# Optimization experiments

Hardware: AMD Instinct MI355X
Metric: run time of the kernel (lower is better)

Reference implementation:

```python
import jax, jax.numpy as jnp
import numpy as np
import math

D_MODEL = 1024
NUM_HEADS = 16
D_K = D_MODEL // NUM_HEADS
MAX_SEQ_LEN = 2048
THETA = 10000.0
BATCH = 2
SEQ = 2048


def setup_inputs() -> dict:
    key = jax.random.key(0)
    ks = jax.random.split(key, 5)
    std = math.sqrt(2.0 / (D_MODEL + D_MODEL))
    def w(k):
        return jnp.clip(std * jax.random.normal(k, (D_MODEL, D_MODEL), dtype=jnp.float32), -3 * std, 3 * std)
    return {
        "x": jax.random.normal(ks[0], (BATCH, SEQ, D_MODEL), dtype=jnp.float32),
        "token_positions": jnp.arange(SEQ, dtype=jnp.int32),
        "Wq": w(ks[1]),
        "Wk": w(ks[2]),
        "Wv": w(ks[3]),
        "Wo": w(ks[4]),
    }


def _rope_tables():
    inv_freq = 1.0 / THETA ** (jnp.arange(0, D_K, 2, dtype=jnp.float32) / D_K)  # [d_k/2]
    positions = jnp.arange(MAX_SEQ_LEN, dtype=jnp.float32)[:, None]             # [max_seq, 1]
    angles = positions * inv_freq                                               # [max_seq, d_k/2]
    return jnp.cos(angles), jnp.sin(angles)


def _apply_rope(x, cos, sin):
    # x: [..., seq, d_k]; cos/sin: [seq, d_k/2] (broadcast over leading dims)
    x1, x2 = x[..., ::2], x[..., 1::2]
    r1 = x1 * cos - x2 * sin
    r2 = x1 * sin + x2 * cos
    return jnp.stack((r1, r2), axis=-1).reshape(x.shape)


def reference(x, token_positions, Wq, Wk, Wv, Wo):
    B, S, D = x.shape
    def proj(W):
        y = jnp.einsum('bsd,od->bso', x, W)
        return y.reshape(B, S, NUM_HEADS, D_K).transpose(0, 2, 1, 3)  # [B,H,S,dk]
    q, k, v = proj(Wq), proj(Wk), proj(Wv)

    cos_t, sin_t = _rope_tables()
    cos, sin = cos_t[token_positions], sin_t[token_positions]  # [S, d_k/2]
    q = _apply_rope(q, cos, sin)
    k = _apply_rope(k, cos, sin)

    scores = jnp.einsum('bhqd,bhkd->bhqk', q, k) / math.sqrt(D_K)
    causal = jnp.tril(jnp.ones((S, S), dtype=bool))
    scores = jnp.where(causal, scores, -jnp.inf)
    attn = jax.nn.softmax(scores, axis=-1)
    out = jnp.einsum('bhqk,bhkd->bhqd', attn, v)
    out = out.transpose(0, 2, 1, 3).reshape(B, S, D)
    return jnp.einsum('bsd,od->bso', out, Wo)
```

## Files before the change

### kernel.cpp

```cpp
#include <hip/hip_runtime.h>
#include <hip/hip_bf16.h>


typedef __attribute__((ext_vector_type(8))) short short8;
typedef __attribute__((ext_vector_type(4))) float floatx4;

static __device__ __forceinline__ unsigned short f2bf(float f) {
  __hip_bfloat16 h = __float2bfloat16(f);
  return *(unsigned short*)&h;
}

static __device__ __forceinline__ unsigned int pk2bf(float a, float b) {
  unsigned int ua = __float_as_uint(a) + 0x8000u;
  unsigned int ub = __float_as_uint(b) + 0x8000u;
  return __builtin_amdgcn_perm(ub, ua, 0x07060302u);
}

static __device__ __forceinline__ float fexp2(float x) {
  float r;
  asm("v_exp_f32 %0, %1\n\ts_nop 0" : "=v"(r) : "v"(x));
  return r;
}

static __device__ __forceinline__ void gl2lds16(const unsigned short* g,
                                                unsigned short* l) {
  __builtin_amdgcn_global_load_lds(
      (const __attribute__((address_space(1))) void*)g,
      (__attribute__((address_space(3))) void*)l, 16, 0, 0);
}

__global__ __launch_bounds__(256) void cvt_all(
    const float4* __restrict__ x,  const float4* __restrict__ wq,
    const float4* __restrict__ wk, const float4* __restrict__ wv,
    const float4* __restrict__ wo,
    ushort4* __restrict__ xb,  ushort4* __restrict__ wqb,
    ushort4* __restrict__ wkb, ushort4* __restrict__ wvb,
    ushort4* __restrict__ wob,
    const int* __restrict__ tokpos,
    float* __restrict__ ctab, float* __restrict__ stab) {
  int t = blockIdx.y;
  int i = blockIdx.x * 256 + threadIdx.x;
  if (t == 5) {
    if (i < 65536) {
      int s = i >> 5, f = i & 31;
      float inv = expf(-9.210340371976184f * (float)(2 * f) / 64.0f);
      float ang = (float)tokpos[s] * inv;
      ctab[i] = cosf(ang);
      stab[i] = sinf(ang);
    }
    return;
  }
  const float4* s = (t == 0) ? x : (t == 1) ? wq : (t == 2) ? wk : (t == 3) ? wv : wo;
  ushort4* d = (t == 0) ? xb : (t == 1) ? wqb : (t == 2) ? wkb : (t == 3) ? wvb : wob;
  int n4 = (t == 0) ? 1048576 : 262144;
  if (i < n4) {
    float4 v = s[i];
    ushort4 o;
    o.x = f2bf(v.x); o.y = f2bf(v.y); o.z = f2bf(v.z); o.w = f2bf(v.w);
    d[i] = o;
  }
}

#define GEMM128_BODY(Aptr, Wptr, m0, n0)                                        \
  __shared__ __align__(16) unsigned short lA[2][128 * 64];                      \
  __shared__ __align__(16) unsigned short lB[2][128 * 64];                      \
  int tid = threadIdx.x;                                                        \
  int wave = tid >> 6, lane = tid & 63;                                         \
  int wm = wave >> 1, wn = wave & 1;                                            \
  int l15 = lane & 15, quad = lane >> 4;                                        \
  int srow = wave * 32 + (lane >> 3);                   \
  int sch = lane & 7;                                   \
  int fsw = l15 & 7;                                 \
  floatx4 acc[4][4];                                                            \
  _Pragma("unroll") for (int m = 0; m < 4; ++m)                                 \
      _Pragma("unroll") for (int n = 0; n < 4; ++n)                             \
          acc[m][n] = (floatx4){0.f, 0.f, 0.f, 0.f};                            \
                    \
  _Pragma("unroll") for (int p = 0; p < 4; ++p) {                               \
    int r = srow + p * 8;                                                       \
    int g = sch ^ (r & 7);                                                      \
    gl2lds16(Aptr + (size_t)(m0 + r) * 1024 + g * 8,                            \
             lA[0] + (wave * 32 + p * 8) * 64);                                 \
    gl2lds16(Wptr + (size_t)(n0 + r) * 1024 + g * 8,                            \
             lB[0] + (wave * 32 + p * 8) * 64);                                 \
  }                                                                             \
  _Pragma("unroll") for (int p = 0; p < 4; ++p) {                               \
    int r = srow + p * 8;                                                       \
    int g = sch ^ (r & 7);                                                      \
    gl2lds16(Aptr + (size_t)(m0 + r) * 1024 + 64 + g * 8,                       \
             lA[1] + (wave * 32 + p * 8) * 64);                                 \
    gl2lds16(Wptr + (size_t)(n0 + r) * 1024 + 64 + g * 8,                       \
             lB[1] + (wave * 32 + p * 8) * 64);                                 \
  }                                                                             \
  asm volatile("s_waitcnt vmcnt(8)" ::: "memory");               \
  __builtin_amdgcn_s_barrier();                                                 \
  for (int kt = 0; kt < 16; ++kt) {                                             \
    int cur = kt & 1;                                                           \
    _Pragma("unroll") for (int ks = 0; ks < 2; ++ks) {                          \
      short8 af[4], bf[4];                                                      \
      _Pragma("unroll") for (int m = 0; m < 4; ++m)                             \
          af[m] = *(const short8*)(lA[cur] + (wm * 64 + m * 16 + l15) * 64 +    \
                                   (((ks * 4 + quad) ^ fsw) * 8));              \
      _Pragma("unroll") for (int n = 0; n < 4; ++n)                             \
          bf[n] = *(const short8*)(lB[cur] + (wn * 64 + n * 16 + l15) * 64 +    \
                                   (((ks * 4 + quad) ^ fsw) * 8));              \
      _Pragma("unroll") for (int m = 0; m < 4; ++m)                             \
          _Pragma("unroll") for (int n = 0; n < 4; ++n)                         \
              acc[m][n] = __builtin_amdgcn_mfma_f32_16x16x32_bf16(              \
                  af[m], bf[n], acc[m][n], 0, 0, 0);                            \
    }                                                                           \
    if (kt == 15) break;                                                        \
    __builtin_amdgcn_s_barrier();                                      \
    if (kt < 14) {                                                              \
      _Pragma("unroll") for (int p = 0; p < 4; ++p) {                           \
        int r = srow + p * 8;                                                   \
        int g = sch ^ (r & 7);                                                  \
        gl2lds16(Aptr + (size_t)(m0 + r) * 1024 + (kt + 2) * 64 + g * 8,        \
                 lA[cur] + (wave * 32 + p * 8) * 64);                           \
        gl2lds16(Wptr + (size_t)(n0 + r) * 1024 + (kt + 2) * 64 + g * 8,        \
                 lB[cur] + (wave * 32 + p * 8) * 64);                           \
      }                                                                         \
      asm volatile("s_waitcnt vmcnt(8)" ::: "memory");        \
    } else {                                                                    \
      asm volatile("s_waitcnt vmcnt(0)" ::: "memory");         \
    }                                                                           \
    __builtin_amdgcn_s_barrier();                                      \
  }

__global__ __launch_bounds__(256) void qkv_mfma(
    const unsigned short* __restrict__ X,
    const unsigned short* __restrict__ Wq,
    const unsigned short* __restrict__ Wk,
    const unsigned short* __restrict__ Wv,
    const float* __restrict__ ctab, const float* __restrict__ stab,
    unsigned short* __restrict__ Qo, unsigned short* __restrict__ Ko,
    unsigned short* __restrict__ Vo) {
  int mat = blockIdx.z;
  const unsigned short* W = (mat == 0) ? Wq : ((mat == 1) ? Wk : Wv);
  unsigned short* Out = (mat == 0) ? Qo : ((mat == 1) ? Ko : Vo);
  int m0 = blockIdx.x * 128, n0 = blockIdx.y * 128;

  GEMM128_BODY(X, W, m0, n0)

#pragma unroll
  for (int n = 0; n < 4; ++n) {
    int col = n0 + wn * 64 + n * 16 + l15;
    int h = col >> 6;
    int d = col & 63;
    int pi = d >> 1;
    bool odd = (d & 1) != 0;
    size_t hb = (size_t)h * 2048 * 64;
#pragma unroll
    for (int m = 0; m < 4; ++m) {
      int row0 = m0 + wm * 64 + m * 16 + quad * 4;
      int b = row0 >> 11;
      int s0 = row0 & 2047;
      size_t base = (size_t)b * 16 * 2048 * 64 + hb;
      if (mat == 2) {
        ushort4 pv;
        pv.x = f2bf(acc[m][n][0]);
        pv.y = f2bf(acc[m][n][1]);
        pv.z = f2bf(acc[m][n][2]);
        pv.w = f2bf(acc[m][n][3]);
        *(ushort4*)(Out + base + (size_t)d * 2048 + s0) = pv;
      } else {
#pragma unroll
        for (int i = 0; i < 4; ++i) {
          int s = s0 + i;
          float v = acc[m][n][i];
          float p = __shfl_xor(v, 1);
          float c = ctab[s * 32 + pi];
          float sn = stab[s * 32 + pi];
          float res = odd ? fmaf(p, sn, v * c) : fmaf(v, c, -p * sn);
          if (mat == 0) res *= 0.1803368801111204f;
          Out[base + (size_t)s * 64 + d] = f2bf(res);
        }
      }
    }
  }
}

__global__ __launch_bounds__(256) void oproj_mfma(
    const unsigned short* __restrict__ A, const unsigned short* __restrict__ Wo,
    float* __restrict__ Out) {
  __shared__ __align__(16) unsigned short lA[2][64 * 64];
  __shared__ __align__(16) unsigned short lB[2][128 * 64];
  int tid = threadIdx.x;
  int wave = tid >> 6, lane = tid & 63;
  int l15 = lane & 15, quad = lane >> 4;
  int rsub = lane >> 3, sch = lane & 7;
  int fsw = l15 & 7;
  int m0 = blockIdx.x * 64, n0 = blockIdx.y * 128;

  floatx4 acc[4][2];
#pragma unroll
  for (int m = 0; m < 4; ++m)
#pragma unroll
    for (int n = 0; n < 2; ++n) acc[m][n] = (floatx4){0.f, 0.f, 0.f, 0.f};

#pragma unroll
  for (int kp = 0; kp < 2; ++kp) {
#pragma unroll
    for (int p = 0; p < 2; ++p) {
      int r = wave * 16 + p * 8 + rsub;
      int g = sch ^ (r & 7);
      gl2lds16(A + (size_t)(m0 + r) * 1024 + kp * 64 + g * 8,
               lA[kp] + (wave * 16 + p * 8) * 64);
    }
#pragma unroll
    for (int p = 0; p < 4; ++p) {
      int r = wave * 32 + p * 8 + rsub;
      int g = sch ^ (r & 7);
      gl2lds16(Wo + (size_t)(n0 + r) * 1024 + kp * 64 + g * 8,
               lB[kp] + (wave * 32 + p * 8) * 64);
    }
  }
  asm volatile("s_waitcnt vmcnt(6)" ::: "memory");
  __builtin_amdgcn_s_barrier();

  for (int kt = 0; kt < 16; ++kt) {
    int cur = kt & 1;
#pragma unroll
    for (int ks = 0; ks < 2; ++ks) {
      int slot = ((ks * 4 + quad) ^ fsw) * 8;
      short8 af[4], bf[2];
#pragma unroll
      for (int m = 0; m < 4; ++m)
        af[m] = *(const short8*)(lA[cur] + (m * 16 + l15) * 64 + slot);
#pragma unroll
      for (int n = 0; n < 2; ++n)
        bf[n] = *(const short8*)(lB[cur] + (wave * 32 + n * 16 + l15) * 64 + slot);
#pragma unroll
      for (int m = 0; m < 4; ++m)
#pragma unroll
        for (int n = 0; n < 2; ++n)
          acc[m][n] = __builtin_amdgcn_mfma_f32_16x16x32_bf16(
              af[m], bf[n], acc[m][n], 0, 0, 0);
    }
    if (kt == 15) break;
    __builtin_amdgcn_s_barrier();
    if (kt < 14) {
#pragma unroll
      for (int p = 0; p < 2; ++p) {
        int r = wave * 16 + p * 8 + rsub;
        int g = sch ^ (r & 7);
        gl2lds16(A + (size_t)(m0 + r) * 1024 + (kt + 2) * 64 + g * 8,
                 lA[cur] + (wave * 16 + p * 8) * 64);
      }
#pragma unroll
      for (int p = 0; p < 4; ++p) {
        int r = wave * 32 + p * 8 + rsub;
        int g = sch ^ (r & 7);
        gl2lds16(Wo + (size_t)(n0 + r) * 1024 + (kt + 2) * 64 + g * 8,
                 lB[cur] + (wave * 32 + p * 8) * 64);
      }
      asm volatile("s_waitcnt vmcnt(6)" ::: "memory");
    } else {
      asm volatile("s_waitcnt vmcnt(0)" ::: "memory");
    }
    __builtin_amdgcn_s_barrier();
  }

#pragma unroll
  for (int m = 0; m < 4; ++m) {
#pragma unroll
    for (int n = 0; n < 2; ++n) {
      int col = n0 + wave * 32 + n * 16 + l15;
#pragma unroll
      for (int i = 0; i < 4; ++i) {
        int row = m0 + m * 16 + quad * 4 + i;
        Out[(size_t)row * 1024 + col] = acc[m][n][i];
      }
    }
  }
}

#define LPS 72

__global__ __launch_bounds__(256) void attn_flash(
    const unsigned short* __restrict__ Q, const unsigned short* __restrict__ K,
    const unsigned short* __restrict__ Vt, unsigned short* __restrict__ Oc) {
  __shared__ __align__(16) unsigned short lK[64 * 64];
  __shared__ __align__(16) unsigned short lV[64 * 64];
  __shared__ unsigned short lP[4][16 * LPS];

  int tid = threadIdx.x;
  int wave = tid >> 6, lane = tid & 63;
  int l15 = lane & 15, quad = lane >> 4;

  int xb_ = blockIdx.x;
  int yb_ = blockIdx.y;
  int jb = yb_ >> 3, ib = yb_ & 7;
  int qtile;
  if (jb == 0)      qtile = xb_;
  else if (jb == 1) qtile = 31 - xb_;
  else if (jb == 2) qtile = (15 - xb_) & 31;
  else              qtile = (16 + xb_) & 31;
  int bh = ib * 4 + jb;

  size_t base = (size_t)bh * 2048 * 64;
  int qbase = qtile * 64;

  const unsigned short* qrow = Q + base + (size_t)(qbase + wave * 16 + l15) * 64;
  short8 qb0 = *(const short8*)(qrow + quad * 8);
  short8 qb1 = *(const short8*)(qrow + 32 + quad * 8);

  floatx4 o[4];
  float m_i = -1e30f, l_i = 0.f;
#pragma unroll
  for (int n = 0; n < 4; ++n) o[n] = (floatx4){0.f, 0.f, 0.f, 0.f};

  int r0 = tid >> 3, g = tid & 7;
  int r1 = r0 + 32;
  int e0 = g * 8;
  int sl = (g ^ (r0 & 7)) * 8;
  int fsw = l15 & 7;
  int c0 = (quad ^ fsw) * 8;
  int c1 = ((quad + 4) ^ fsw) * 8;

  const unsigned short* kp = K + base;
  const unsigned short* vp = Vt + base;
  short8 pk0 = *(const short8*)(kp + r0 * 64 + e0);
  short8 pk1 = *(const short8*)(kp + r1 * 64 + e0);
  short8 pv0 = *(const short8*)(vp + (size_t)r0 * 2048 + e0);
  short8 pv1 = *(const short8*)(vp + (size_t)r1 * 2048 + e0);

  for (int kt = 0; kt <= qtile; ++kt) {
    __syncthreads();
    *(short8*)(lK + r0 * 64 + sl) = pk0;
    *(short8*)(lK + r1 * 64 + sl) = pk1;
    *(short8*)(lV + r0 * 64 + sl) = pv0;
    *(short8*)(lV + r1 * 64 + sl) = pv1;
    __syncthreads();

    if (kt < qtile) {
      const unsigned short* kn = K + base + (size_t)(kt + 1) * 4096;
      const unsigned short* vn = Vt + base + (kt + 1) * 64;
      pk0 = *(const short8*)(kn + r0 * 64 + e0);
      pk1 = *(const short8*)(kn + r1 * 64 + e0);
      pv0 = *(const short8*)(vn + (size_t)r0 * 2048 + e0);
      pv1 = *(const short8*)(vn + (size_t)r1 * 2048 + e0);
    }

    float sc[4][4];
#pragma unroll
    for (int sub = 0; sub < 4; ++sub) {
      const unsigned short* kr = lK + (sub * 16 + l15) * 64;
      short8 a0 = *(const short8*)(kr + c0);
      short8 a1 = *(const short8*)(kr + c1);
      floatx4 s = {0.f, 0.f, 0.f, 0.f};
      s = __builtin_amdgcn_mfma_f32_16x16x32_bf16(a0, qb0, s, 0, 0, 0);
      s = __builtin_amdgcn_mfma_f32_16x16x32_bf16(a1, qb1, s, 0, 0, 0);
#pragma unroll
      for (int i = 0; i < 4; ++i) sc[sub][i] = s[i];
    }

    if (kt == qtile) {
      int qin = wave * 16 + l15;
#pragma unroll
      for (int sub = 0; sub < 4; ++sub)
#pragma unroll
        for (int i = 0; i < 4; ++i)
          if (sub * 16 + quad * 4 + i > qin) sc[sub][i] = -1e30f;
    }

    float mb = sc[0][0];
#pragma unroll
    for (int sub = 0; sub < 4; ++sub)
#pragma unroll
      for (int i = 0; i < 4; ++i) mb = fmaxf(mb, sc[sub][i]);
    mb = fmaxf(mb, __shfl_xor(mb, 16));
    mb = fmaxf(mb, __shfl_xor(mb, 32));

    float mn = fmaxf(m_i, mb);
    float al = fexp2(m_i - mn);
    m_i = mn;
    float rs = 0.f;
#pragma unroll
    for (int sub = 0; sub < 4; ++sub)
#pragma unroll
      for (int i = 0; i < 4; ++i) {
        float p = fexp2(sc[sub][i] - mn);
        sc[sub][i] = p;
        rs += p;
      }
    rs += __shfl_xor(rs, 16);
    rs += __shfl_xor(rs, 32);
    l_i = l_i * al + rs;

#pragma unroll
    for (int n = 0; n < 4; ++n) {
      o[n][0] *= al; o[n][1] *= al; o[n][2] *= al; o[n][3] *= al;
    }

    unsigned short* pw = lP[wave] + l15 * LPS;
#pragma unroll
    for (int sub = 0; sub < 4; ++sub) {
      uint2 w;
      w.x = pk2bf(sc[sub][0], sc[sub][1]);
      w.y = pk2bf(sc[sub][2], sc[sub][3]);
      *(uint2*)(pw + sub * 16 + quad * 4) = w;
    }

    const unsigned short* pr = lP[wave] + l15 * LPS + quad * 8;
    short8 pa0 = *(const short8*)(pr);
    short8 pa1 = *(const short8*)(pr + 32);

#pragma unroll
    for (int n = 0; n < 4; ++n) {
      const unsigned short* vr = lV + (n * 16 + l15) * 64;
      short8 vb0 = *(const short8*)(vr + c0);
      short8 vb1 = *(const short8*)(vr + c1);
      o[n] = __builtin_amdgcn_mfma_f32_16x16x32_bf16(vb0, pa0, o[n], 0, 0, 0);
      o[n] = __builtin_amdgcn_mfma_f32_16x16x32_bf16(vb1, pa1, o[n], 0, 0, 0);
    }
  }

  int b = bh >> 4, h = bh & 15;
  float inv = 1.f / l_i;
  int s = qbase + wave * 16 + l15;
  size_t orow = (size_t)(b * 2048 + s) * 1024 + h * 64;
#pragma unroll
  for (int n = 0; n < 4; ++n) {
    uint2 ov;
    ov.x = pk2bf(o[n][0] * inv, o[n][1] * inv);
    ov.y = pk2bf(o[n][2] * inv, o[n][3] * inv);
    *(uint2*)(Oc + orow + n * 16 + quad * 4) = ov;
  }
}

extern "C" void kernel_launch(void* const* d_in, const int* in_sizes, int n_in,
                              void* d_out, int out_size, void* d_ws, size_t ws_size,
                              hipStream_t stream) {
  const float* x  = (const float*)d_in[0];
  const int* tokpos = (const int*)d_in[1];
  const float* Wq = (const float*)d_in[2];
  const float* Wk = (const float*)d_in[3];
  const float* Wv = (const float*)d_in[4];
  const float* Wo = (const float*)d_in[5];
  float* out = (float*)d_out;

  float* ws = (float*)d_ws;
  float* ctab = ws;
  float* stab = ctab + 65536;
  unsigned short* u = (unsigned short*)(stab + 65536);
  unsigned short* Qb  = u;
  unsigned short* Kb  = Qb + 4194304;
  unsigned short* Vb  = Kb + 4194304;
  unsigned short* Oc  = Vb + 4194304;
  unsigned short* xb  = Oc + 4194304;
  unsigned short* Wqb = xb + 4194304;
  unsigned short* Wkb = Wqb + 1048576;
  unsigned short* Wvb = Wkb + 1048576;
  unsigned short* Wob = Wvb + 1048576;

  cvt_all<<<dim3(4096, 6), 256, 0, stream>>>(
      (const float4*)x, (const float4*)Wq, (const float4*)Wk,
      (const float4*)Wv, (const float4*)Wo,
      (ushort4*)xb, (ushort4*)Wqb, (ushort4*)Wkb, (ushort4*)Wvb, (ushort4*)Wob,
      tokpos, ctab, stab);

  qkv_mfma<<<dim3(32, 8, 3), 256, 0, stream>>>(
      xb, Wqb, Wkb, Wvb, ctab, stab, Qb, Kb, Vb);
  attn_flash<<<dim3(32, 32), 256, 0, stream>>>(Qb, Kb, Vb, Oc);
  oproj_mfma<<<dim3(64, 8), 256, 0, stream>>>(Oc, Wob, out);
}
```

Measured before the change: 186.3 us.

## Pair complementary causal query tiles per attention block to share K/V loads

Each attention block now processes two query tiles, tA and 31-tA, that share the same (batch, head). The K/V tiles staged in LDS are reused by both, and every block does the same total amount of causal work. The grid shrinks from 1024 blocks to 512, and launch bounds now request 2 blocks per SM. In exchange, register pressure roughly doubles because two sets of accumulators and Q fragments are live, and parallelism drops to 512 blocks.

```diff
diff --git a/kernel.cpp b/kernel.cpp
--- a/kernel.cpp
+++ b/kernel.cpp
@@ -277,38 +277,119 @@
 
 #define LPS 72
 
-__global__ __launch_bounds__(256) void attn_flash(
+static __device__ __forceinline__ void qk_step(
+    const unsigned short* lK, int l15, int c0, int c1,
+    short8 q0, short8 q1, floatx4 (&sc)[4]) {
+#pragma unroll
+  for (int sub = 0; sub < 4; ++sub) {
+    const unsigned short* kr = lK + (sub * 16 + l15) * 64;
+    short8 a0 = *(const short8*)(kr + c0);
+    short8 a1 = *(const short8*)(kr + c1);
+    floatx4 s = {0.f, 0.f, 0.f, 0.f};
+    s = __builtin_amdgcn_mfma_f32_16x16x32_bf16(a0, q0, s, 0, 0, 0);
+    s = __builtin_amdgcn_mfma_f32_16x16x32_bf16(a1, q1, s, 0, 0, 0);
+    sc[sub] = s;
+  }
+}
+
+static __device__ __forceinline__ void sm_step(
+    floatx4 (&sc)[4], float& m_i, float& l_i, floatx4 (&o)[4],
+    bool diag, int qin, int quad) {
+  if (diag) {
+#pragma unroll
+    for (int sub = 0; sub < 4; ++sub)
+#pragma unroll
+      for (int i = 0; i < 4; ++i)
+        if (sub * 16 + quad * 4 + i > qin) sc[sub][i] = -1e30f;
+  }
+  float mb = sc[0][0];
+#pragma unroll
+  for (int sub = 0; sub < 4; ++sub)
+#pragma unroll
+    for (int i = 0; i < 4; ++i) mb = fmaxf(mb, sc[sub][i]);
+  mb = fmaxf(mb, __shfl_xor(mb, 16));
+  mb = fmaxf(mb, __shfl_xor(mb, 32));
+
+  float mn = fmaxf(m_i, mb);
+  float al = fexp2(m_i - mn);
+  m_i = mn;
+  float rs = 0.f;
+#pragma unroll
+  for (int sub = 0; sub < 4; ++sub)
+#pragma unroll
+    for (int i = 0; i < 4; ++i) {
+      float p = fexp2(sc[sub][i] - mn);
+      sc[sub][i] = p;
+      rs += p;
+    }
+  rs += __shfl_xor(rs, 16);
+  rs += __shfl_xor(rs, 32);
+  l_i = l_i * al + rs;
+#pragma unroll
+  for (int n = 0; n < 4; ++n) {
+    o[n][0] *= al; o[n][1] *= al; o[n][2] *= al; o[n][3] *= al;
+  }
+}
+
+static __device__ __forceinline__ void pv_step(
+    const floatx4 (&sc)[4], floatx4 (&o)[4], unsigned short* lPw,
+    const unsigned short* lV, int l15, int quad, int c0, int c1) {
+  unsigned short* pw = lPw + l15 * LPS;
+#pragma unroll
+  for (int sub = 0; sub < 4; ++sub) {
+    uint2 w;
+    w.x = pk2bf(sc[sub][0], sc[sub][1]);
+    w.y = pk2bf(sc[sub][2], sc[sub][3]);
+    *(uint2*)(pw + sub * 16 + quad * 4) = w;
+  }
+  const unsigned short* pr = lPw + l15 * LPS + quad * 8;
+  short8 pa0 = *(const short8*)(pr);
+  short8 pa1 = *(const short8*)(pr + 32);
+#pragma unroll
+  for (int n = 0; n < 4; ++n) {
+    const unsigned short* vr = lV + (n * 16 + l15) * 64;
+    short8 vb0 = *(const short8*)(vr + c0);
+    short8 vb1 = *(const short8*)(vr + c1);
+    o[n] = __builtin_amdgcn_mfma_f32_16x16x32_bf16(vb0, pa0, o[n], 0, 0, 0);
+    o[n] = __builtin_amdgcn_mfma_f32_16x16x32_bf16(vb1, pa1, o[n], 0, 0, 0);
+  }
+}
+
+__global__ __launch_bounds__(256, 2) void attn_flash(
     const unsigned short* __restrict__ Q, const unsigned short* __restrict__ K,
     const unsigned short* __restrict__ Vt, unsigned short* __restrict__ Oc) {
   __shared__ __align__(16) unsigned short lK[64 * 64];
   __shared__ __align__(16) unsigned short lV[64 * 64];
-  __shared__ unsigned short lP[4][16 * LPS];
+  __shared__ unsigned short lP[8][16 * LPS];
 
   int tid = threadIdx.x;
   int wave = tid >> 6, lane = tid & 63;
   int l15 = lane & 15, quad = lane >> 4;
 
-  int xb_ = blockIdx.x;
-  int yb_ = blockIdx.y;
-  int jb = yb_ >> 3, ib = yb_ & 7;
-  int qtile;
-  if (jb == 0)      qtile = xb_;
-  else if (jb == 1) qtile = 31 - xb_;
-  else if (jb == 2) qtile = (15 - xb_) & 31;
-  else              qtile = (16 + xb_) & 31;
-  int bh = ib * 4 + jb;
+  int id = blockIdx.x;
+  int rest = id >> 3;
+  int pair = rest >> 2;
+  int bh = (id & 7) * 4 + (rest & 3);
+  int tA = pair;
+  int tB = 31 - pair;
+  int NT = tB + 1;
 
   size_t base = (size_t)bh * 2048 * 64;
-  int qbase = qtile * 64;
-
-  const unsigned short* qrow = Q + base + (size_t)(qbase + wave * 16 + l15) * 64;
-  short8 qb0 = *(const short8*)(qrow + quad * 8);
-  short8 qb1 = *(const short8*)(qrow + 32 + quad * 8);
-
-  floatx4 o[4];
-  float m_i = -1e30f, l_i = 0.f;
-#pragma unroll
-  for (int n = 0; n < 4; ++n) o[n] = (floatx4){0.f, 0.f, 0.f, 0.f};
+
+  const unsigned short* qrowA = Q + base + (size_t)(tA * 64 + wave * 16 + l15) * 64;
+  const unsigned short* qrowB = Q + base + (size_t)(tB * 64 + wave * 16 + l15) * 64;
+  short8 qA0 = *(const short8*)(qrowA + quad * 8);
+  short8 qA1 = *(const short8*)(qrowA + 32 + quad * 8);
+  short8 qB0 = *(const short8*)(qrowB + quad * 8);
+  short8 qB1 = *(const short8*)(qrowB + 32 + quad * 8);
+
+  floatx4 oA[4], oB[4];
+  float mA_i = -1e30f, lA_i = 0.f, mB_i = -1e30f, lB_i = 0.f;
+#pragma unroll
+  for (int n = 0; n < 4; ++n) {
+    oA[n] = (floatx4){0.f, 0.f, 0.f, 0.f};
+    oB[n] = (floatx4){0.f, 0.f, 0.f, 0.f};
+  }
 
   int r0 = tid >> 3, g = tid & 7;
   int r1 = r0 + 32;
@@ -325,7 +406,11 @@
   short8 pv0 = *(const short8*)(vp + (size_t)r0 * 2048 + e0);
   short8 pv1 = *(const short8*)(vp + (size_t)r1 * 2048 + e0);
 
-  for (int kt = 0; kt <= qtile; ++kt) {
+  int qin = wave * 16 + l15;
+
+  for (int kt = 0; kt < NT; ++kt) {
+    bool aAct = (kt <= tA);
+
     __syncthreads();
     *(short8*)(lK + r0 * 64 + sl) = pk0;
     *(short8*)(lK + r1 * 64 + sl) = pk1;
@@ -333,7 +418,7 @@
     *(short8*)(lV + r1 * 64 + sl) = pv1;
     __syncthreads();
 
-    if (kt < qtile) {
+    if (kt + 1 < NT) {
       const unsigned short* kn = K + base + (size_t)(kt + 1) * 4096;
       const unsigned short* vn = Vt + base + (kt + 1) * 64;
       pk0 = *(const short8*)(kn + r0 * 64 + e0);
@@ -342,90 +427,41 @@
       pv1 = *(const short8*)(vn + (size_t)r1 * 2048 + e0);
     }
 
-    float sc[4][4];
-#pragma unroll
-    for (int sub = 0; sub < 4; ++sub) {
-      const unsigned short* kr = lK + (sub * 16 + l15) * 64;
-      short8 a0 = *(const short8*)(kr + c0);
-      short8 a1 = *(const short8*)(kr + c1);
-      floatx4 s = {0.f, 0.f, 0.f, 0.f};
-      s = __builtin_amdgcn_mfma_f32_16x16x32_bf16(a0, qb0, s, 0, 0, 0);
-      s = __builtin_amdgcn_mfma_f32_16x16x32_bf16(a1, qb1, s, 0, 0, 0);
-#pragma unroll
-      for (int i = 0; i < 4; ++i) sc[sub][i] = s[i];
-    }
-
-    if (kt == qtile) {
-      int qin = wave * 16 + l15;
-#pragma unroll
-      for (int sub = 0; sub < 4; ++sub)
-#pragma unroll
-        for (int i = 0; i < 4; ++i)
-          if (sub * 16 + quad * 4 + i > qin) sc[sub][i] = -1e30f;
-    }
-
-    float mb = sc[0][0];
-#pragma unroll
-    for (int sub = 0; sub < 4; ++sub)
-#pragma unroll
-      for (int i = 0; i < 4; ++i) mb = fmaxf(mb, sc[sub][i]);
-    mb = fmaxf(mb, __shfl_xor(mb, 16));
-    mb = fmaxf(mb, __shfl_xor(mb, 32));
-
-    float mn = fmaxf(m_i, mb);
-    float al = fexp2(m_i - mn);
-    m_i = mn;
-    float rs = 0.f;
-#pragma unroll
-    for (int sub = 0; sub < 4; ++sub)
-#pragma unroll
-      for (int i = 0; i < 4; ++i) {
-        float p = fexp2(sc[sub][i] - mn);
-        sc[sub][i] = p;
-        rs += p;
-      }
-    rs += __shfl_xor(rs, 16);
-    rs += __shfl_xor(rs, 32);
-    l_i = l_i * al + rs;
-
+    floatx4 scB[4], scA[4];
+    qk_step(lK, l15, c0, c1, qB0, qB1, scB);
+    if (aAct) qk_step(lK, l15, c0, c1, qA0, qA1, scA);
+
+    sm_step(scB, mB_i, lB_i, oB, kt == NT - 1, qin, quad);
+    if (aAct) sm_step(scA, mA_i, lA_i, oA, kt == tA, qin, quad);
+
+    pv_step(scB, oB, lP[wave * 2], lV, l15, quad, c0, c1);
+    if (aAct) pv_step(scA, oA, lP[wave * 2 + 1], lV, l15, quad, c0, c1);
+  }
+
+  int b = bh >> 4, h = bh & 15;
+  {
+    float inv = 1.f / lB_i;
+    int s = tB * 64 + wave * 16 + l15;
+    size_t orow = (size_t)(b * 2048 + s) * 1024 + h * 64;
 #pragma unroll
     for (int n = 0; n < 4; ++n) {
-      o[n][0] *= al; o[n][1] *= al; o[n][2] *= al; o[n][3] *= al;
-    }
-
-    unsigned short* pw = lP[wave] + l15 * LPS;
-#pragma unroll
-    for (int sub = 0; sub < 4; ++sub) {
-      uint2 w;
-      w.x = pk2bf(sc[sub][0], sc[sub][1]);
-      w.y = pk2bf(sc[sub][2], sc[sub][3]);
-      *(uint2*)(pw + sub * 16 + quad * 4) = w;
-    }
-
-    const unsigned short* pr = lP[wave] + l15 * LPS + quad * 8;
-    short8 pa0 = *(const short8*)(pr);
-    short8 pa1 = *(const short8*)(pr + 32);
-
+      uint2 ov;
+      ov.x = pk2bf(oB[n][0] * inv, oB[n][1] * inv);
+      ov.y = pk2bf(oB[n][2] * inv, oB[n][3] * inv);
+      *(uint2*)(Oc + orow + n * 16 + quad * 4) = ov;
+    }
+  }
+  {
+    float inv = 1.f / lA_i;
+    int s = tA * 64 + wave * 16 + l15;
+    size_t orow = (size_t)(b * 2048 + s) * 1024 + h * 64;
 #pragma unroll
     for (int n = 0; n < 4; ++n) {
-      const unsigned short* vr = lV + (n * 16 + l15) * 64;
-      short8 vb0 = *(const short8*)(vr + c0);
-      short8 vb1 = *(const short8*)(vr + c1);
-      o[n] = __builtin_amdgcn_mfma_f32_16x16x32_bf16(vb0, pa0, o[n], 0, 0, 0);
-      o[n] = __builtin_amdgcn_mfma_f32_16x16x32_bf16(vb1, pa1, o[n], 0, 0, 0);
-    }
-  }
-
-  int b = bh >> 4, h = bh & 15;
-  float inv = 1.f / l_i;
-  int s = qbase + wave * 16 + l15;
-  size_t orow = (size_t)(b * 2048 + s) * 1024 + h * 64;
-#pragma unroll
-  for (int n = 0; n < 4; ++n) {
-    uint2 ov;
-    ov.x = pk2bf(o[n][0] * inv, o[n][1] * inv);
-    ov.y = pk2bf(o[n][2] * inv, o[n][3] * inv);
-    *(uint2*)(Oc + orow + n * 16 + quad * 4) = ov;
+      uint2 ov;
+      ov.x = pk2bf(oA[n][0] * inv, oA[n][1] * inv);
+      ov.y = pk2bf(oA[n][2] * inv, oA[n][3] * inv);
+      *(uint2*)(Oc + orow + n * 16 + quad * 4) = ov;
+    }
   }
 }
 
@@ -462,6 +498,6 @@
 
   qkv_mfma<<<dim3(32, 8, 3), 256, 0, stream>>>(
       xb, Wqb, Wkb, Wvb, ctab, stab, Qb, Kb, Vb);
-  attn_flash<<<dim3(32, 32), 256, 0, stream>>>(Qb, Kb, Vb, Oc);
+  attn_flash<<<dim3(512), 256, 0, stream>>>(Qb, Kb, Vb, Oc);
   oproj_mfma<<<dim3(64, 8), 256, 0, stream>>>(Oc, Wob, out);
 }
```

Result: faster. 179.7 us (-3.6%).
